# Performance work log

Measured on AMD Instinct MI355X. Metric: run time of the kernel, lower is better.

Reference implementation:

```python
import jax, jax.numpy as jnp
import numpy as np

PATCH_SIZE = 14
MERGE = 2  # spatial_merge_size
D = 1024
B = 8
IMG_PX = 1792  # 128 patches per side


def setup_inputs() -> dict:
    key = jax.random.key(0)
    k1, k2 = jax.random.split(key)
    n_patches_per_img = (IMG_PX // PATCH_SIZE) ** 2  # 16384
    total = B * n_patches_per_img                    # 131072
    image_features = jax.random.normal(k1, (1, total, D), dtype=jnp.float32)
    image_sizes = jnp.full((B, 2), IMG_PX, dtype=jnp.int32)
    # nn.Linear(D*MERGE**2, D, bias=False): weight (D, D*MERGE**2), y = x @ W.T
    W = jax.random.normal(k2, (D, D * MERGE * MERGE), dtype=jnp.float32) * (1.0 / np.sqrt(D * MERGE * MERGE))
    return {"image_features": image_features, "image_sizes": image_sizes, "W": W}


def _merge_one(xi, h, w, S):
    # xi: (h*w, D) in row-major (h, w) patch order
    d = xi.shape[-1]
    x = xi.reshape(h // S, S, w // S, S, d)
    # -> (h/S, w/S, D, S, S): matches torch unfold channel-major (d, ki, kj) column order
    x = x.transpose(0, 2, 4, 1, 3)
    return x.reshape((h // S) * (w // S), d * S * S)


def reference(image_features, image_sizes, W):
    sizes = np.asarray(image_sizes)  # static per-image pixel sizes
    x = image_features[0]  # (sum N_i, D)
    S = MERGE
    blocks = []
    off = 0
    for h_px, w_px in sizes:  # loop over B images (small, structurally distinct shapes)
        h, w = int(h_px) // PATCH_SIZE, int(w_px) // PATCH_SIZE
        n = h * w
        blocks.append(_merge_one(jax.lax.dynamic_slice_in_dim(x, off, n, axis=0), h, w, S))
        off += n
    merged = jnp.concatenate(blocks, axis=0)            # (sum L_i, D*S^2)
    out = jnp.einsum('nk,dk->nd', merged, W)            # single global GEMM
    return out[None, :, :]                              # (1, sum L_i, D)
```

## Files before the change

### kernel.cpp

```cpp
#include <hip/hip_runtime.h>
#include <hip/hip_bf16.h>
#include <stdint.h>


#define M_TOTAL 32768
#define K_DIM   4096
#define N_DIM   1024
#define BM 128
#define BN 128
#define BK 64
#define LP 72

typedef __attribute__((ext_vector_type(8))) short short8;
typedef __attribute__((ext_vector_type(4))) float f32x4;
typedef __attribute__((ext_vector_type(8))) unsigned short us8;

static __device__ __forceinline__ unsigned pack2bf(float lo, float hi) {
    unsigned a = __builtin_bit_cast(unsigned, lo) + 0x8000u;
    unsigned b = __builtin_bit_cast(unsigned, hi) + 0x8000u;
    return __builtin_amdgcn_perm(b, a, 0x07060302);
}

__global__ __launch_bounds__(256) void repack_w(const float* __restrict__ W,
                                                unsigned short* __restrict__ Wp) {
    int t = blockIdx.x * 256 + threadIdx.x;
    int j  = t >> 8;
    int d0 = (t & 255) << 2;
    const float4* src = (const float4*)(W + (size_t)j * K_DIM + (size_t)d0 * 4);
    float4 v0 = src[0], v1 = src[1], v2 = src[2], v3 = src[3];
    float vs[4][4] = {{v0.x, v1.x, v2.x, v3.x},
                      {v0.y, v1.y, v2.y, v3.y},
                      {v0.z, v1.z, v2.z, v3.z},
                      {v0.w, v1.w, v2.w, v3.w}};
#pragma unroll
    for (int s = 0; s < 4; s++) {
        uint2 o;
        o.x = pack2bf(vs[s][0], vs[s][1]);
        o.y = pack2bf(vs[s][2], vs[s][3]);
        *(uint2*)(Wp + (size_t)j * K_DIM + s * 1024 + d0) = o;
    }
}

__global__ __launch_bounds__(256) void merge_gemm(
        const float* __restrict__ X,
        const unsigned short* __restrict__ Wp,
        float* __restrict__ out) {
    __shared__ unsigned short As[BM][LP];
    __shared__ unsigned short Bs[BN][LP];

    const int tid  = threadIdx.x;
    const int lane = tid & 63;
    const int wave = tid >> 6;
    const int wm   = (wave >> 1) * 64;
    const int wn   = (wave & 1) * 64;
    const int lrow = lane & 15;
    const int quad = lane >> 4;

    const int blk = blockIdx.x;
    const int bn  = (blk & 7) * BN;
    const int bm  = (blk >> 3) * BM;

    const int arow = tid >> 4;
    const int acol = (tid & 15) << 2;

    const float* abase[8];
#pragma unroll
    for (int rep = 0; rep < 8; rep++) {
        int m   = bm + arow + rep * 16;
        int img = m >> 12;
        int r   = m & 4095;
        int bi  = r >> 6;
        int bj  = r & 63;
        int pbase = img * 16384 + bi * 256 + bj * 2;
        abase[rep] = X + (size_t)pbase * 1024 + acol;
    }

    const int brow = tid >> 3;
    const int bcol = (tid & 7) << 3;

    f32x4 acc[4][4] = {};

    for (int k0 = 0; k0 < K_DIM; k0 += BK) {
        const int s    = k0 >> 10;
        const int d0   = k0 & 1023;
        const int aoff = (((s >> 1) * 128) + (s & 1)) * 1024 + d0;

#pragma unroll
        for (int rep = 0; rep < 8; rep++) {
            const float4 v = *(const float4*)(abase[rep] + aoff);
            uint2 o;
            o.x = pack2bf(v.x, v.y);
            o.y = pack2bf(v.z, v.w);
            *(uint2*)&As[arow + rep * 16][acol] = o;
        }
#pragma unroll
        for (int rep = 0; rep < 4; rep++) {
            us8 v = *(const us8*)(Wp + (size_t)(bn + brow + rep * 32) * K_DIM + k0 + bcol);
            *(us8*)&Bs[brow + rep * 32][bcol] = v;
        }
        __syncthreads();

#pragma unroll
        for (int kk = 0; kk < 2; kk++) {
            const int koff = kk * 32 + quad * 8;
            short8 a[4], b[4];
#pragma unroll
            for (int i = 0; i < 4; i++)
                a[i] = *(const short8*)&As[wm + i * 16 + lrow][koff];
#pragma unroll
            for (int j = 0; j < 4; j++)
                b[j] = *(const short8*)&Bs[wn + j * 16 + lrow][koff];
#pragma unroll
            for (int i = 0; i < 4; i++)
#pragma unroll
                for (int j = 0; j < 4; j++)
                    acc[i][j] = __builtin_amdgcn_mfma_f32_16x16x32_bf16(
                        a[i], b[j], acc[i][j], 0, 0, 0);
        }
        __syncthreads();
    }

    const int ocol = bn + wn + lrow;
#pragma unroll
    for (int i = 0; i < 4; i++) {
#pragma unroll
        for (int r = 0; r < 4; r++) {
            float* po = out + (size_t)(bm + wm + i * 16 + quad * 4 + r) * N_DIM + ocol;
#pragma unroll
            for (int j = 0; j < 4; j++)
                po[j * 16] = acc[i][j][r];
        }
    }
}

extern "C" void kernel_launch(void* const* d_in, const int* in_sizes, int n_in,
                              void* d_out, int out_size, void* d_ws, size_t ws_size,
                              hipStream_t stream) {
    const float* X = (const float*)d_in[0];
    const float* W = (const float*)d_in[2];
    float* out = (float*)d_out;
    unsigned short* Wp = (unsigned short*)d_ws;

    repack_w<<<dim3(1024), dim3(256), 0, stream>>>(W, Wp);
    merge_gemm<<<dim3((M_TOTAL / BM) * (N_DIM / BN)), dim3(256), 0, stream>>>(X, Wp, out);
}
```

Measured before the change: 1.149 ms.

## Pre-gather activations to bf16 buffer and use async LDS loads in GEMM

Adds a separate pass that gathers the 2x2 merged patches and converts them to bf16 into a workspace buffer. A new GEMM kernel then loads contiguous bf16 tiles of A and W straight into shared memory with global_load_lds and reads them through an XOR-swizzled layout. The intent is to remove the fp32 gather and conversion from the GEMM inner loop and cut its global traffic. The cost is an extra pass over the activations and 256MB of workspace, and it falls back to the old kernel if the workspace is too small.

```diff
diff --git a/kernel.cpp b/kernel.cpp
--- a/kernel.cpp
+++ b/kernel.cpp
@@ -9,11 +9,15 @@
 #define BM 128
 #define BN 128
 #define BK 64
-#define LP 72
 
 typedef __attribute__((ext_vector_type(8))) short short8;
 typedef __attribute__((ext_vector_type(4))) float f32x4;
 typedef __attribute__((ext_vector_type(8))) unsigned short us8;
+
+#define ASYNC_COPY16(gsrc, ldst)                                                     \
+    __builtin_amdgcn_global_load_lds(                                                \
+        (const __attribute__((address_space(1))) unsigned int*)(const void*)(gsrc),  \
+        (__attribute__((address_space(3))) unsigned int*)(ldst), 16, 0, 0)
 
 static __device__ __forceinline__ unsigned pack2bf(float lo, float hi) {
     unsigned a = __builtin_bit_cast(unsigned, lo) + 0x8000u;
@@ -41,6 +45,105 @@
     }
 }
 
+__global__ __launch_bounds__(256) void gather_convert(const float* __restrict__ X,
+                                                      unsigned short* __restrict__ Ap) {
+    int idx = blockIdx.x * 256 + threadIdx.x;
+    int p   = idx >> 6;
+    int c16 = (idx & 63) << 4;
+    int img = p >> 14;
+    int r   = p & 16383;
+    int pi  = r >> 7;
+    int pj  = r & 127;
+    int m   = img * 4096 + (pi >> 1) * 64 + (pj >> 1);
+    int s   = ((pi & 1) << 1) | (pj & 1);
+    const float4* src = (const float4*)(X + (size_t)p * 1024 + c16);
+    float4 v0 = src[0], v1 = src[1], v2 = src[2], v3 = src[3];
+    uint4 o0, o1;
+    o0.x = pack2bf(v0.x, v0.y); o0.y = pack2bf(v0.z, v0.w);
+    o0.z = pack2bf(v1.x, v1.y); o0.w = pack2bf(v1.z, v1.w);
+    o1.x = pack2bf(v2.x, v2.y); o1.y = pack2bf(v2.z, v2.w);
+    o1.z = pack2bf(v3.x, v3.y); o1.w = pack2bf(v3.z, v3.w);
+    uint4* dst = (uint4*)(Ap + (size_t)m * K_DIM + s * 1024 + c16);
+    dst[0] = o0;
+    dst[1] = o1;
+}
+
+__global__ __launch_bounds__(256) void gemm_bt(
+        const unsigned short* __restrict__ Ap,
+        const unsigned short* __restrict__ Wp,
+        float* __restrict__ out) {
+    __shared__ unsigned short As[BM * BK];
+    __shared__ unsigned short Bs[BN * BK];
+
+    const int tid  = threadIdx.x;
+    const int lane = tid & 63;
+    const int wave = tid >> 6;
+    const int wm   = (wave >> 1) * 64;
+    const int wn   = (wave & 1) * 64;
+    const int lrow = lane & 15;
+    const int quad = lane >> 4;
+
+    const int blk = blockIdx.x;
+    const int bn  = (blk & 7) * BN;
+    const int bm  = (blk >> 3) * BM;
+
+    const int rowoff = lane >> 3;
+    const int cswz   = (lane & 7) ^ rowoff;
+    const unsigned short* agp =
+        Ap + (size_t)(bm + wave * 32 + rowoff) * K_DIM + cswz * 8;
+    const unsigned short* bgp =
+        Wp + (size_t)(bn + wave * 32 + rowoff) * K_DIM + cswz * 8;
+    unsigned short* alp = As + (wave * 32) * BK;
+    unsigned short* blp = Bs + (wave * 32) * BK;
+
+    f32x4 acc[4][4] = {};
+
+    for (int k0 = 0; k0 < K_DIM; k0 += BK) {
+#pragma unroll
+        for (int i = 0; i < 4; i++) {
+            ASYNC_COPY16(agp + i * 8 * K_DIM + k0, alp + i * 8 * BK);
+            ASYNC_COPY16(bgp + i * 8 * K_DIM + k0, blp + i * 8 * BK);
+        }
+        __syncthreads();
+
+#pragma unroll
+        for (int kk = 0; kk < 2; kk++) {
+            const int c0 = kk * 4 + quad;
+            short8 a[4], b[4];
+#pragma unroll
+            for (int i = 0; i < 4; i++) {
+                const int ar = wm + i * 16 + lrow;
+                a[i] = *(const short8*)&As[ar * BK + ((c0 ^ (lrow & 7)) << 3)];
+            }
+#pragma unroll
+            for (int j = 0; j < 4; j++) {
+                const int br = wn + j * 16 + lrow;
+                b[j] = *(const short8*)&Bs[br * BK + ((c0 ^ (lrow & 7)) << 3)];
+            }
+#pragma unroll
+            for (int i = 0; i < 4; i++)
+#pragma unroll
+                for (int j = 0; j < 4; j++)
+                    acc[i][j] = __builtin_amdgcn_mfma_f32_16x16x32_bf16(
+                        a[i], b[j], acc[i][j], 0, 0, 0);
+        }
+        __syncthreads();
+    }
+
+    const int ocol = bn + wn + lrow;
+#pragma unroll
+    for (int i = 0; i < 4; i++) {
+#pragma unroll
+        for (int r = 0; r < 4; r++) {
+            float* po = out + (size_t)(bm + wm + i * 16 + quad * 4 + r) * N_DIM + ocol;
+#pragma unroll
+            for (int j = 0; j < 4; j++)
+                po[j * 16] = acc[i][j][r];
+        }
+    }
+}
+
+#define LP 72
 __global__ __launch_bounds__(256) void merge_gemm(
         const float* __restrict__ X,
         const unsigned short* __restrict__ Wp,
@@ -139,8 +242,18 @@
     const float* X = (const float*)d_in[0];
     const float* W = (const float*)d_in[2];
     float* out = (float*)d_out;
+
     unsigned short* Wp = (unsigned short*)d_ws;
+    const size_t WP_BYTES = (size_t)N_DIM * K_DIM * 2;
+    const size_t AP_BYTES = (size_t)M_TOTAL * K_DIM * 2;
 
     repack_w<<<dim3(1024), dim3(256), 0, stream>>>(W, Wp);
-    merge_gemm<<<dim3((M_TOTAL / BM) * (N_DIM / BN)), dim3(256), 0, stream>>>(X, Wp, out);
-}
+
+    if (ws_size >= WP_BYTES + AP_BYTES) {
+        unsigned short* Ap = (unsigned short*)((char*)d_ws + WP_BYTES);
+        gather_convert<<<dim3(32768), dim3(256), 0, stream>>>(X, Ap);
+        gemm_bt<<<dim3((M_TOTAL / BM) * (N_DIM / BN)), dim3(256), 0, stream>>>(Ap, Wp, out);
+    } else {
+        merge_gemm<<<dim3((M_TOTAL / BM) * (N_DIM / BN)), dim3(256), 0, stream>>>(X, Wp, out);
+    }
+}
```

After: 1.049 ms. 8.7% less time.
